# Performance work log

Measured on AMD Instinct MI355X. Metric: run time of the kernel, lower is better.

Reference implementation:

```python
import jax, jax.numpy as jnp
import numpy as np
import math

B, T, D, H = 8, 1024, 512, 8
DK = D // H


def setup_inputs() -> dict:
    key = jax.random.key(0)
    ks = jax.random.split(key, 16)
    f = lambda k, s: jax.random.normal(k, s, dtype=jnp.float32)
    p = lambda k, s: jax.random.normal(k, s, dtype=jnp.float32) * 0.02
    return {
        "query": f(ks[0], (B, T, D)),
        "key": f(ks[1], (B, T, D)),
        "value": f(ks[2], (B, T, D)),
        "pos_embedding": f(ks[3], (B, T, D)),
        "Wq": p(ks[4], (D, D)), "bq": p(ks[5], (D,)),
        "Wk": p(ks[6], (D, D)), "bk": p(ks[7], (D,)),
        "Wv": p(ks[8], (D, D)), "bv": p(ks[9], (D,)),
        "Wp": p(ks[10], (D, D)),
        "u_bias": p(ks[11], (H, DK)),
        "v_bias": p(ks[12], (H, DK)),
        "Wo": p(ks[13], (D, D)), "bo": p(ks[14], (D,)),
    }


def _rel_shift(pos_score):
    # pos_score: [B, H, T, T]  -> Transformer-XL relative shift via pad/reshape
    b, h, t1, t2 = pos_score.shape
    padded = jnp.concatenate(
        [jnp.zeros((b, h, t1, 1), pos_score.dtype), pos_score], axis=-1
    )  # [B,H,T,T+1]
    padded = padded.reshape(b, h, t2 + 1, t1)
    return padded[:, :, 1:].reshape(b, h, t1, t2)


def reference(query, key, value, pos_embedding, Wq, bq, Wk, bk, Wv, bv, Wp,
              u_bias, v_bias, Wo, bo):
    q = (query @ Wq + bq).reshape(B, T, H, DK)          # [B,T,H,DK]
    k = (key @ Wk + bk).reshape(B, T, H, DK)
    v = (value @ Wv + bv).reshape(B, T, H, DK)
    p = (pos_embedding @ Wp).reshape(B, T, H, DK)

    content_score = jnp.einsum("bihd,bjhd->bhij", q + u_bias, k)
    pos_score = jnp.einsum("bihd,bjhd->bhij", q + v_bias, p)
    pos_score = _rel_shift(pos_score)

    score = (content_score + pos_score) / math.sqrt(D)  # note: sqrt(d_model)
    attn = jax.nn.softmax(score, axis=-1)               # dropout: eval mode
    context = jnp.einsum("bhij,bjhd->bihd", attn, v).reshape(B, T, D)
    return context @ Wo + bo
```

## Files before the change

kernel.cpp:

```cpp
#include <hip/hip_runtime.h>

#define B_ 8
#define T_ 1024
#define D_ 512
#define H_ 8
#define DK_ 64

typedef __bf16 bf16x8 __attribute__((ext_vector_type(8)));
typedef float f32x4 __attribute__((ext_vector_type(4)));

#define MFMA16(a, b, c) __builtin_amdgcn_mfma_f32_16x16x32_bf16(a, b, c, 0, 0, 0)

__device__ __forceinline__ bf16x8 pack8(float4 a, float4 b) {
  bf16x8 r;
  r[0] = (__bf16)a.x; r[1] = (__bf16)a.y; r[2] = (__bf16)a.z; r[3] = (__bf16)a.w;
  r[4] = (__bf16)b.x; r[5] = (__bf16)b.y; r[6] = (__bf16)b.z; r[7] = (__bf16)b.w;
  return r;
}

__device__ __forceinline__ void load_lds16(const void* g, void* l) {
  __builtin_amdgcn_global_load_lds(
      (const __attribute__((address_space(1))) void*)g,
      (__attribute__((address_space(3))) void*)l, 16, 0, 0);
}

__global__ __launch_bounds__(256) void cvt_x(const float* __restrict__ q,
                                             const float* __restrict__ k,
                                             const float* __restrict__ v,
                                             const float* __restrict__ p,
                                             __bf16* __restrict__ dst) {
  const float* src = (blockIdx.y == 0) ? q
                   : (blockIdx.y == 1) ? k
                   : (blockIdx.y == 2) ? v : p;
  const size_t e = ((size_t)blockIdx.x * 256 + threadIdx.x) * 8;
  const int row = (int)(e >> 9);
  const int kk = (int)(e & 511);
  const int phys = (kk & ~63) | ((((kk >> 3) & 7) ^ (row & 7)) << 3);
  float4 a = *(const float4*)(src + e);
  float4 b = *(const float4*)(src + e + 4);
  *(bf16x8*)(dst + (size_t)blockIdx.y * 4194304 + (size_t)row * 512 + phys) =
      pack8(a, b);
}

__global__ __launch_bounds__(256) void cvt_w(const float* __restrict__ w0,
                                             const float* __restrict__ w1,
                                             const float* __restrict__ w2,
                                             const float* __restrict__ w3,
                                             const float* __restrict__ w4,
                                             __bf16* __restrict__ wt) {
  __shared__ float Ts[64][65];
  const float* W = (blockIdx.z == 0) ? w0
                 : (blockIdx.z == 1) ? w1
                 : (blockIdx.z == 2) ? w2
                 : (blockIdx.z == 3) ? w3 : w4;
  const int tid = threadIdx.x;
  const int kt = blockIdx.x * 64, nt = blockIdx.y * 64;
  const int r = tid >> 2, co = (tid & 3) * 16;
#pragma unroll
  for (int q = 0; q < 4; ++q)
    *(float4*)&Ts[r][co + q * 4] =
        *(const float4*)(W + (size_t)(kt + r) * 512 + nt + co + q * 4);
  __syncthreads();
  bf16x8 o0, o1;
#pragma unroll
  for (int q = 0; q < 8; ++q) o0[q] = (__bf16)Ts[co + q][r];
#pragma unroll
  for (int q = 0; q < 8; ++q) o1[q] = (__bf16)Ts[co + 8 + q][r];
  const int key = r & 7;
  __bf16* dst =
      wt + (size_t)blockIdx.z * 262144 + (size_t)(nt + r) * 512 + kt;
  *(bf16x8*)(dst + (((co >> 3) ^ key) << 3)) = o0;
  *(bf16x8*)(dst + ((((co >> 3) + 1) ^ key) << 3)) = o1;
}

template <int PHASE>
__global__ __launch_bounds__(256, 4) void gemm_dma(
    const __bf16* __restrict__ Xc, const __bf16* __restrict__ ctxA,
    const __bf16* __restrict__ Wt, const float* __restrict__ bq,
    const float* __restrict__ bk, const float* __restrict__ bv,
    const float* __restrict__ bo, const float* __restrict__ u,
    const float* __restrict__ v, __bf16* __restrict__ quB,
    __bf16* __restrict__ qvB, __bf16* __restrict__ kB,
    __bf16* __restrict__ vT, __bf16* __restrict__ pB,
    float* __restrict__ out) {
  __shared__ __bf16 smem[17408];
  __bf16* As = smem;
  __bf16* Bs = smem + 8192;
  const int tid = threadIdx.x;
  const int z = blockIdx.z;
  const int wave = tid >> 6, lane = tid & 63, l16 = lane & 15, quad = lane >> 4;
  const int wm = wave & 1, wn = wave >> 1;
  const int m0 = blockIdx.x * 128, n0 = blockIdx.y * 128;

  const __bf16* Ag = PHASE ? ctxA : Xc + (size_t)z * (8192 * 512);
  const __bf16* Bg = Wt + (size_t)(PHASE ? 4 : z) * (512 * 512);

  const int drow = tid >> 3, dch = (tid & 7) * 8;
  char* ldsA = (char*)As + (tid & 192) * 16;
  char* ldsB = (char*)Bs + (tid & 192) * 16;
  const int keyc = l16 & 7;

  f32x4 acc[4][4];
#pragma unroll
  for (int rb = 0; rb < 4; ++rb)
#pragma unroll
    for (int cb = 0; cb < 4; ++cb) acc[rb][cb] = 0.f;

#pragma unroll 1
  for (int k0 = 0; k0 < 512; k0 += 64) {
    __syncthreads();
#pragma unroll
    for (int c4 = 0; c4 < 4; ++c4) {
      load_lds16(Ag + (size_t)(m0 + c4 * 32 + drow) * 512 + k0 + dch,
                 ldsA + c4 * 4096);
      load_lds16(Bg + (size_t)(n0 + c4 * 32 + drow) * 512 + k0 + dch,
                 ldsB + c4 * 4096);
    }
    __syncthreads();
#pragma unroll
    for (int s = 0; s < 2; ++s) {
      const int ph = ((s * 4 + quad) ^ keyc) << 3;
      bf16x8 afr[4], bfr[4];
#pragma unroll
      for (int rb = 0; rb < 4; ++rb)
        afr[rb] = *(const bf16x8*)&As[(wm * 64 + rb * 16 + l16) * 64 + ph];
#pragma unroll
      for (int cb = 0; cb < 4; ++cb)
        bfr[cb] = *(const bf16x8*)&Bs[(wn * 64 + cb * 16 + l16) * 64 + ph];
#pragma unroll
      for (int rb = 0; rb < 4; ++rb)
#pragma unroll
        for (int cb = 0; cb < 4; ++cb)
          acc[rb][cb] = MFMA16(afr[rb], bfr[cb], acc[rb][cb]);
    }
  }

  if (PHASE == 1) {
#pragma unroll
    for (int rb = 0; rb < 4; ++rb)
#pragma unroll
      for (int cb = 0; cb < 4; ++cb) {
        const int col = n0 + wn * 64 + cb * 16 + l16;
        const float bb = bo[col];
#pragma unroll
        for (int r = 0; r < 4; ++r) {
          const int row = m0 + wm * 64 + rb * 16 + quad * 4 + r;
          out[(size_t)row * 512 + col] = acc[rb][cb][r] + bb;
        }
      }
    return;
  }

  if (z == 2) {
    __syncthreads();
    __bf16* Tt = smem;
#pragma unroll
    for (int rb = 0; rb < 4; ++rb)
#pragma unroll
      for (int cb = 0; cb < 4; ++cb) {
        const int cl = wn * 64 + cb * 16 + l16;
        const float bb = bv[n0 + cl];
#pragma unroll
        for (int r = 0; r < 4; ++r) {
          const int rl = wm * 64 + rb * 16 + quad * 4 + r;
          Tt[cl * 136 + rl] = (__bf16)(acc[rb][cb][r] + bb);
        }
      }
    __syncthreads();
    const int r2 = tid >> 1, ch = (tid & 1) * 64;
    const int hh = (n0 + r2) >> 6, dkk = (n0 + r2) & 63;
    const int bI = m0 >> 10, t0 = m0 & 1023;
    __bf16* dst = vT + (((size_t)(bI * H_ + hh)) * DK_ + dkk) * T_ + t0 + ch;
#pragma unroll
    for (int q = 0; q < 8; ++q)
      *(bf16x8*)(dst + q * 8) = *(const bf16x8*)&Tt[r2 * 136 + ch + q * 8];
    return;
  }

#pragma unroll
  for (int rb = 0; rb < 4; ++rb)
#pragma unroll
    for (int cb = 0; cb < 4; ++cb) {
      const int col = n0 + wn * 64 + cb * 16 + l16;
      const float bb = (z == 0) ? bq[col] : (z == 1) ? bk[col] : 0.f;
      const float uu = (z == 0) ? u[col] : 0.f;
      const float vv = (z == 0) ? v[col] : 0.f;
#pragma unroll
      for (int r = 0; r < 4; ++r) {
        const int row = m0 + wm * 64 + rb * 16 + quad * 4 + r;
        const float val = acc[rb][cb][r] + bb;
        const int bI = row >> 10, tt = row & 1023;
        const int hh = col >> 6, dk = col & 63;
        const size_t idx = (((size_t)(bI * H_ + hh)) * T_ + tt) * DK_ + dk;
        if (z == 0) {
          quB[idx] = (__bf16)(val + uu);
          qvB[idx] = (__bf16)(val + vv);
        } else if (z == 1) {
          kB[idx] = (__bf16)val;
        } else {
          pB[idx] = (__bf16)val;
        }
      }
    }
}

__global__ __launch_bounds__(256, 3) void attn_mfma(
    const __bf16* __restrict__ qu, const __bf16* __restrict__ qv,
    const __bf16* __restrict__ kbuf, const __bf16* __restrict__ vT,
    const __bf16* __restrict__ pbuf, __bf16* __restrict__ ctx) {
  constexpr float SCALE = 0.044194173824159216f;
  __shared__ __bf16 Kt[64 * 72];
  __shared__ __bf16 Vt[64 * 72];
  __shared__ __bf16 Pb[128 * 72];
  __bf16* Rs = Kt;

  const int tid = threadIdx.x;
  const int wave = tid >> 6, lane = tid & 63, l16 = lane & 15, quad = lane >> 4;
  const int g = blockIdx.x;
  const int bhq = (g & 7) * 8 + (g >> 7);
  const int i0 = ((g >> 3) & 15) * 64;
  const size_t bh = (size_t)bhq * T_ * DK_;
  const __bf16* QU = qu + bh;
  const __bf16* QV = qv + bh;
  const __bf16* Kg = kbuf + bh;
  const __bf16* Vg = vT + bh;
  const __bf16* Pg = pbuf + bh;

  bf16x8 quA[2], qvw[2], qv4[2];
  {
    const int rw = i0 + wave * 16 + l16;
    const int r4g = i0 + 64 + l16;
    const int r4 = (r4g < T_) ? r4g : T_ - 1;
#pragma unroll
    for (int s = 0; s < 2; ++s) {
      const int ko = s * 32 + quad * 8;
      quA[s] = *(const bf16x8*)&QU[(size_t)rw * DK_ + ko];
      qvw[s] = *(const bf16x8*)&QV[(size_t)rw * DK_ + ko];
      qv4[s] = *(const bf16x8*)&QV[(size_t)r4 * DK_ + ko];
    }
  }

  f32x4 Oacc[4];
#pragma unroll
  for (int cb = 0; cb < 4; ++cb) Oacc[cb] = 0.f;
  float lrun[4];
#pragma unroll
  for (int r = 0; r < 4; ++r) lrun[r] = 0.f;

  const int rbase = wave * 16 + quad * 4;
  const int kr = tid >> 2, kko = (tid & 3) * 16;
  const int vd = tid >> 2, vjo = (tid & 3) * 16;
  const int po = tid >> 1, pko = (tid & 1) * 32;

  bf16x8 kpre[2], vpre[2], ppre[4];
#define LOAD_KVP(JT)                                                          \
  {                                                                           \
    const int j0_ = (JT) * 64;                                                \
    const __bf16* ks_ = Kg + (size_t)(j0_ + kr) * DK_ + kko;                  \
    kpre[0] = *(const bf16x8*)ks_;                                            \
    kpre[1] = *(const bf16x8*)(ks_ + 8);                                      \
    const __bf16* vs_ = Vg + (size_t)vd * T_ + j0_ + vjo;                     \
    vpre[0] = *(const bf16x8*)vs_;                                            \
    vpre[1] = *(const bf16x8*)(vs_ + 8);                                      \
    int cs_ = T_ - 65 + j0_ - i0;                                             \
    if (cs_ < 0) cs_ += T_;                                                   \
    if (cs_ >= T_) cs_ -= T_;                                                 \
    int prow_ = cs_ + po;                                                     \
    if (prow_ >= T_) prow_ -= T_;                                             \
    const __bf16* ps_ = Pg + (size_t)prow_ * DK_ + pko;                       \
    ppre[0] = *(const bf16x8*)ps_;                                            \
    ppre[1] = *(const bf16x8*)(ps_ + 8);                                      \
    ppre[2] = *(const bf16x8*)(ps_ + 16);                                     \
    ppre[3] = *(const bf16x8*)(ps_ + 24);                                     \
  }

  LOAD_KVP(0)

#pragma unroll 1
  for (int jt = 0; jt < 16; ++jt) {
    const int j0 = jt * 64;
    __syncthreads();
    *(bf16x8*)&Kt[kr * 72 + kko] = kpre[0];
    *(bf16x8*)&Kt[kr * 72 + kko + 8] = kpre[1];
    *(bf16x8*)&Vt[vd * 72 + vjo] = vpre[0];
    *(bf16x8*)&Vt[vd * 72 + vjo + 8] = vpre[1];
    *(bf16x8*)&Pb[po * 72 + pko] = ppre[0];
    *(bf16x8*)&Pb[po * 72 + pko + 8] = ppre[1];
    *(bf16x8*)&Pb[po * 72 + pko + 16] = ppre[2];
    *(bf16x8*)&Pb[po * 72 + pko + 24] = ppre[3];
    __syncthreads();
    if (jt < 15) LOAD_KVP(jt + 1)

    f32x4 sA[4];
#pragma unroll
    for (int cb = 0; cb < 4; ++cb) sA[cb] = 0.f;
#pragma unroll
    for (int s = 0; s < 2; ++s)
#pragma unroll
      for (int cb = 0; cb < 4; ++cb) {
        bf16x8 kf = *(const bf16x8*)&Kt[(cb * 16 + l16) * 72 + s * 32 + quad * 8];
        sA[cb] = MFMA16(quA[s], kf, sA[cb]);
      }

    __syncthreads();

#pragma unroll
    for (int c = 0; c < 5; ++c) {
      const int cb = 3 - wave + c;
      f32x4 rc = 0.f;
#pragma unroll
      for (int s = 0; s < 2; ++s) {
        bf16x8 pf = *(const bf16x8*)&Pb[(cb * 16 + l16) * 72 + s * 32 + quad * 8];
        rc = MFMA16(qvw[s], pf, rc);
      }
      const int col = cb * 16 + l16;
#pragma unroll
      for (int rr = 0; rr < 4; ++rr) {
        const int dj = col + rbase + rr - 64;
        if (dj >= 0 && dj < 64) Rs[(rbase + rr) * 68 + dj] = (__bf16)rc[rr];
      }
    }
    {
      const int cb = wave;
      f32x4 rc = 0.f;
#pragma unroll
      for (int s = 0; s < 2; ++s) {
        bf16x8 pf = *(const bf16x8*)&Pb[(cb * 16 + l16) * 72 + s * 32 + quad * 8];
        rc = MFMA16(qv4[s], pf, rc);
      }
      if (quad == 0) Rs[64 * 68 + cb * 16 + l16] = (__bf16)rc[0];
    }
    __syncthreads();

    __bf16* Pa = Pb;
#pragma unroll
    for (int r = 0; r < 4; ++r) {
#pragma unroll
      for (int cb = 0; cb < 4; ++cb) {
        const int di = rbase + r;
        const int dj = cb * 16 + l16;
        const int ji = (j0 + dj) - (i0 + di);
        float pos = 0.f;
        if (ji != 1) pos = (float)Rs[(di + (ji >= 2 ? 1 : 0)) * 68 + dj];
        const float w_ = __expf((sA[cb][r] + pos) * SCALE);
        lrun[r] += w_;
        Pa[di * 68 + dj] = (__bf16)w_;
      }
    }

#pragma unroll
    for (int s = 0; s < 2; ++s) {
      bf16x8 ap = *(const bf16x8*)&Pa[(wave * 16 + l16) * 68 + s * 32 + quad * 8];
#pragma unroll
      for (int cb = 0; cb < 4; ++cb) {
        bf16x8 bv = *(const bf16x8*)&Vt[(cb * 16 + l16) * 72 + s * 32 + quad * 8];
        Oacc[cb] = MFMA16(ap, bv, Oacc[cb]);
      }
    }
  }

  float inv[4];
#pragma unroll
  for (int r = 0; r < 4; ++r) {
    float L = lrun[r];
    L += __shfl_xor(L, 1);
    L += __shfl_xor(L, 2);
    L += __shfl_xor(L, 4);
    L += __shfl_xor(L, 8);
    inv[r] = 1.f / L;
  }
  const int b = bhq >> 3, h = bhq & 7;
#pragma unroll
  for (int cb = 0; cb < 4; ++cb)
#pragma unroll
    for (int r = 0; r < 4; ++r) {
      const int row = i0 + rbase + r;
      const int chunk = cb * 2 + (l16 >> 3);
      const int col = h * DK_ + ((chunk ^ (row & 7)) << 3) + (l16 & 7);
      ctx[((size_t)(b * T_ + row)) * D_ + col] = (__bf16)(Oacc[cb][r] * inv[r]);
    }
}

extern "C" void kernel_launch(void* const* d_in, const int* in_sizes, int n_in,
                              void* d_out, int out_size, void* d_ws,
                              size_t ws_size, hipStream_t stream) {
  const float* query = (const float*)d_in[0];
  const float* key   = (const float*)d_in[1];
  const float* value = (const float*)d_in[2];
  const float* pos   = (const float*)d_in[3];
  const float* Wq = (const float*)d_in[4];
  const float* bq = (const float*)d_in[5];
  const float* Wk = (const float*)d_in[6];
  const float* bk = (const float*)d_in[7];
  const float* Wv = (const float*)d_in[8];
  const float* bv = (const float*)d_in[9];
  const float* Wp = (const float*)d_in[10];
  const float* ub = (const float*)d_in[11];
  const float* vbias = (const float*)d_in[12];
  const float* Wo = (const float*)d_in[13];
  const float* bo = (const float*)d_in[14];
  float* out = (float*)d_out;

  char* ws = (char*)d_ws;
  const size_t ACT = (size_t)8192 * 512 * 2;
  __bf16* Xc  = (__bf16*)ws;
  __bf16* quB = (__bf16*)(ws + 4 * ACT);
  __bf16* qvB = (__bf16*)(ws + 5 * ACT);
  __bf16* kB  = (__bf16*)(ws + 6 * ACT);
  __bf16* pB  = (__bf16*)(ws + 7 * ACT);
  __bf16* vT  = (__bf16*)(ws + 8 * ACT);
  __bf16* Wt  = (__bf16*)(ws + 9 * ACT);
  __bf16* ctx = Xc;

  cvt_x<<<dim3(2048, 4), 256, 0, stream>>>(query, key, value, pos, Xc);
  cvt_w<<<dim3(8, 8, 5), 256, 0, stream>>>(Wq, Wk, Wv, Wp, Wo, Wt);

  gemm_dma<0><<<dim3(64, 4, 4), 256, 0, stream>>>(
      Xc, nullptr, Wt, bq, bk, bv, bo, ub, vbias, quB, qvB, kB, vT, pB,
      nullptr);

  attn_mfma<<<dim3(1024), 256, 0, stream>>>(quB, qvB, kB, vT, pB, ctx);

  gemm_dma<1><<<dim3(64, 4, 1), 256, 0, stream>>>(
      nullptr, ctx, Wt, bq, bk, bv, bo, ub, vbias, quB, qvB, kB, vT, pB,
      out);
}
```

Baseline: 277.7 us.

## Load K/V/P tiles directly to LDS with XOR-swizzled global layouts

```diff
diff --git a/kernel.cpp b/kernel.cpp
--- a/kernel.cpp
+++ b/kernel.cpp
@@ -171,9 +171,10 @@
     const int hh = (n0 + r2) >> 6, dkk = (n0 + r2) & 63;
     const int bI = m0 >> 10, t0 = m0 & 1023;
     __bf16* dst = vT + (((size_t)(bI * H_ + hh)) * DK_ + dkk) * T_ + t0 + ch;
+    const int vkey = dkk & 7;
 #pragma unroll
     for (int q = 0; q < 8; ++q)
-      *(bf16x8*)(dst + q * 8) = *(const bf16x8*)&Tt[r2 * 136 + ch + q * 8];
+      *(bf16x8*)(dst + ((q ^ vkey) * 8)) = *(const bf16x8*)&Tt[r2 * 136 + ch + q * 8];
     return;
   }
 
@@ -191,7 +192,10 @@
         const float val = acc[rb][cb][r] + bb;
         const int bI = row >> 10, tt = row & 1023;
         const int hh = col >> 6, dk = col & 63;
-        const size_t idx = (((size_t)(bI * H_ + hh)) * T_ + tt) * DK_ + dk;
+        const int dks = (z == 0)
+            ? dk
+            : ((dk & 7) | ((((dk >> 3) ^ tt) & 7) << 3));
+        const size_t idx = (((size_t)(bI * H_ + hh)) * T_ + tt) * DK_ + dks;
         if (z == 0) {
           quB[idx] = (__bf16)(val + uu);
           qvB[idx] = (__bf16)(val + vv);
@@ -204,15 +208,17 @@
     }
 }
 
-__global__ __launch_bounds__(256, 3) void attn_mfma(
+__global__ __launch_bounds__(256, 4) void attn_mfma(
     const __bf16* __restrict__ qu, const __bf16* __restrict__ qv,
     const __bf16* __restrict__ kbuf, const __bf16* __restrict__ vT,
     const __bf16* __restrict__ pbuf, __bf16* __restrict__ ctx) {
   constexpr float SCALE = 0.044194173824159216f;
-  __shared__ __bf16 Kt[64 * 72];
-  __shared__ __bf16 Vt[64 * 72];
-  __shared__ __bf16 Pb[128 * 72];
-  __bf16* Rs = Kt;
+  __shared__ __bf16 smemA[4488];
+  __shared__ __bf16 Vt[4096];
+  __shared__ __bf16 Pb[8192];
+  __bf16* Kt = smemA;
+  __bf16* Rs = smemA;
+  __bf16* Pa = Pb;
 
   const int tid = threadIdx.x;
   const int wave = tid >> 6, lane = tid & 63, l16 = lane & 15, quad = lane >> 4;
@@ -248,48 +254,33 @@
   for (int r = 0; r < 4; ++r) lrun[r] = 0.f;
 
   const int rbase = wave * 16 + quad * 4;
-  const int kr = tid >> 2, kko = (tid & 3) * 16;
-  const int vd = tid >> 2, vjo = (tid & 3) * 16;
-  const int po = tid >> 1, pko = (tid & 1) * 32;
-
-  bf16x8 kpre[2], vpre[2], ppre[4];
-#define LOAD_KVP(JT)                                                          \
-  {                                                                           \
-    const int j0_ = (JT) * 64;                                                \
-    const __bf16* ks_ = Kg + (size_t)(j0_ + kr) * DK_ + kko;                  \
-    kpre[0] = *(const bf16x8*)ks_;                                            \
-    kpre[1] = *(const bf16x8*)(ks_ + 8);                                      \
-    const __bf16* vs_ = Vg + (size_t)vd * T_ + j0_ + vjo;                     \
-    vpre[0] = *(const bf16x8*)vs_;                                            \
-    vpre[1] = *(const bf16x8*)(vs_ + 8);                                      \
-    int cs_ = T_ - 65 + j0_ - i0;                                             \
-    if (cs_ < 0) cs_ += T_;                                                   \
-    if (cs_ >= T_) cs_ -= T_;                                                 \
-    int prow_ = cs_ + po;                                                     \
-    if (prow_ >= T_) prow_ -= T_;                                             \
-    const __bf16* ps_ = Pg + (size_t)prow_ * DK_ + pko;                       \
-    ppre[0] = *(const bf16x8*)ps_;                                            \
-    ppre[1] = *(const bf16x8*)(ps_ + 8);                                      \
-    ppre[2] = *(const bf16x8*)(ps_ + 16);                                     \
-    ppre[3] = *(const bf16x8*)(ps_ + 24);                                     \
-  }
-
-  LOAD_KVP(0)
+  const int keyr = l16 & 7;
+  const int keyp = (l16 + 7) & 7;
+  const int drow = tid >> 3;
+  const int dch = (tid & 7) * 8;
+  char* ldsK = (char*)Kt + (tid & 192) * 16;
+  char* ldsV = (char*)Vt + (tid & 192) * 16;
+  char* ldsP = (char*)Pb + (tid & 192) * 16;
 
 #pragma unroll 1
   for (int jt = 0; jt < 16; ++jt) {
     const int j0 = jt * 64;
-    __syncthreads();
-    *(bf16x8*)&Kt[kr * 72 + kko] = kpre[0];
-    *(bf16x8*)&Kt[kr * 72 + kko + 8] = kpre[1];
-    *(bf16x8*)&Vt[vd * 72 + vjo] = vpre[0];
-    *(bf16x8*)&Vt[vd * 72 + vjo + 8] = vpre[1];
-    *(bf16x8*)&Pb[po * 72 + pko] = ppre[0];
-    *(bf16x8*)&Pb[po * 72 + pko + 8] = ppre[1];
-    *(bf16x8*)&Pb[po * 72 + pko + 16] = ppre[2];
-    *(bf16x8*)&Pb[po * 72 + pko + 24] = ppre[3];
-    __syncthreads();
-    if (jt < 15) LOAD_KVP(jt + 1)
+    int cs = T_ - 65 + j0 - i0;
+    if (cs < 0) cs += T_;
+    if (cs >= T_) cs -= T_;
+
+    __syncthreads();
+    load_lds16(Kg + (size_t)(j0 + drow) * 64 + dch, ldsK);
+    load_lds16(Kg + (size_t)(j0 + 32 + drow) * 64 + dch, ldsK + 4096);
+    load_lds16(Vg + (size_t)drow * T_ + j0 + dch, ldsV);
+    load_lds16(Vg + (size_t)(32 + drow) * T_ + j0 + dch, ldsV + 4096);
+#pragma unroll
+    for (int c = 0; c < 4; ++c) {
+      int prow = cs + c * 32 + drow;
+      if (prow >= T_) prow -= T_;
+      load_lds16(Pg + (size_t)prow * 64 + dch, ldsP + c * 4096);
+    }
+    __syncthreads();
 
     f32x4 sA[4];
 #pragma unroll
@@ -298,7 +289,8 @@
     for (int s = 0; s < 2; ++s)
 #pragma unroll
       for (int cb = 0; cb < 4; ++cb) {
-        bf16x8 kf = *(const bf16x8*)&Kt[(cb * 16 + l16) * 72 + s * 32 + quad * 8];
+        bf16x8 kf = *(const bf16x8*)&Kt[(cb * 16 + l16) * 64 +
+                                        (((s * 4 + quad) ^ keyr) << 3)];
         sA[cb] = MFMA16(quA[s], kf, sA[cb]);
       }
 
@@ -310,7 +302,8 @@
       f32x4 rc = 0.f;
 #pragma unroll
       for (int s = 0; s < 2; ++s) {
-        bf16x8 pf = *(const bf16x8*)&Pb[(cb * 16 + l16) * 72 + s * 32 + quad * 8];
+        bf16x8 pf = *(const bf16x8*)&Pb[(cb * 16 + l16) * 64 +
+                                        (((s * 4 + quad) ^ keyp) << 3)];
         rc = MFMA16(qvw[s], pf, rc);
       }
       const int col = cb * 16 + l16;
@@ -325,14 +318,14 @@
       f32x4 rc = 0.f;
 #pragma unroll
       for (int s = 0; s < 2; ++s) {
-        bf16x8 pf = *(const bf16x8*)&Pb[(cb * 16 + l16) * 72 + s * 32 + quad * 8];
+        bf16x8 pf = *(const bf16x8*)&Pb[(cb * 16 + l16) * 64 +
+                                        (((s * 4 + quad) ^ keyp) << 3)];
         rc = MFMA16(qv4[s], pf, rc);
       }
       if (quad == 0) Rs[64 * 68 + cb * 16 + l16] = (__bf16)rc[0];
     }
     __syncthreads();
 
-    __bf16* Pa = Pb;
 #pragma unroll
     for (int r = 0; r < 4; ++r) {
 #pragma unroll
@@ -344,16 +337,18 @@
         if (ji != 1) pos = (float)Rs[(di + (ji >= 2 ? 1 : 0)) * 68 + dj];
         const float w_ = __expf((sA[cb][r] + pos) * SCALE);
         lrun[r] += w_;
-        Pa[di * 68 + dj] = (__bf16)w_;
+        Pa[di * 64 + (dj & 7) + ((((dj >> 3) ^ di) & 7) << 3)] = (__bf16)w_;
       }
     }
 
 #pragma unroll
     for (int s = 0; s < 2; ++s) {
-      bf16x8 ap = *(const bf16x8*)&Pa[(wave * 16 + l16) * 68 + s * 32 + quad * 8];
+      bf16x8 ap = *(const bf16x8*)&Pa[(wave * 16 + l16) * 64 +
+                                      (((s * 4 + quad) ^ keyr) << 3)];
 #pragma unroll
       for (int cb = 0; cb < 4; ++cb) {
-        bf16x8 bv = *(const bf16x8*)&Vt[(cb * 16 + l16) * 72 + s * 32 + quad * 8];
+        bf16x8 bv = *(const bf16x8*)&Vt[(cb * 16 + l16) * 64 +
+                                        (((s * 4 + quad) ^ keyr) << 3)];
         Oacc[cb] = MFMA16(ap, bv, Oacc[cb]);
       }
     }
```

New measurement: 257.5 us. 7.2% less time.
